# Kernel tuning notes

Measured on AMD Instinct MI355X. Metric: run time of the kernel, lower is better.

The kernel has to match this reference:

```python
import jax, jax.numpy as jnp
import numpy as np
from jax import lax

INPUT, HIDDEN, OUT = 64, 128, 40
B, T = 256, 512


def _lstm_layer(x, Wih, Whh, bih, bhh):
    # x: [B, T, D]; PyTorch gate order: i, f, g, o in stacked [4H, .] weights
    Bsz = x.shape[0]
    H = Whh.shape[1]
    b = bih + bhh

    def step(carry, xt):
        h, c = carry
        gates = xt @ Wih.T + h @ Whh.T + b  # [B, 4H]
        i, f, g, o = jnp.split(gates, 4, axis=-1)
        i = jax.nn.sigmoid(i)
        f = jax.nn.sigmoid(f)
        g = jnp.tanh(g)
        o = jax.nn.sigmoid(o)
        c = f * c + i * g
        h = o * jnp.tanh(c)
        return (h, c), h

    init = (jnp.zeros((Bsz, H), x.dtype), jnp.zeros((Bsz, H), x.dtype))
    (h_last, _), ys = lax.scan(step, init, jnp.swapaxes(x, 0, 1))
    return jnp.swapaxes(ys, 0, 1), h_last


def setup_inputs() -> dict:
    key = jax.random.key(0)
    ks = jax.random.split(key, 11)
    s_in = 1.0 / np.sqrt(HIDDEN)
    u = lambda k, shp: jax.random.uniform(k, shp, jnp.float32, -s_in, s_in)
    return {
        "x": jax.random.normal(ks[0], (B, T, INPUT), jnp.float32),
        "Wih0": u(ks[1], (4 * HIDDEN, INPUT)),
        "Whh0": u(ks[2], (4 * HIDDEN, HIDDEN)),
        "bih0": u(ks[3], (4 * HIDDEN,)),
        "bhh0": u(ks[4], (4 * HIDDEN,)),
        "Wih1": u(ks[5], (4 * HIDDEN, HIDDEN)),
        "Whh1": u(ks[6], (4 * HIDDEN, HIDDEN)),
        "bih1": u(ks[7], (4 * HIDDEN,)),
        "bhh1": u(ks[8], (4 * HIDDEN,)),
        "Wfc": u(ks[9], (OUT, HIDDEN)),
        "bfc": u(ks[10], (OUT,)),
    }


def reference(x, Wih0, Whh0, bih0, bhh0, Wih1, Whh1, bih1, bhh1, Wfc, bfc):
    y0, _ = _lstm_layer(x, Wih0, Whh0, bih0, bhh0)        # [B, T, H]
    _, h_last = _lstm_layer(y0, Wih1, Whh1, bih1, bhh1)   # [B, H] == y[:, -1]
    return h_last @ Wfc.T + bfc                            # [B, 40]
```

## Files before the change

kernel.cpp:

```cpp
#include <hip/hip_runtime.h>

#define BATCH 256
#define TLEN  512
#define DIN   64
#define HID   128
#define NOUT  40

typedef _Float16 f16x8 __attribute__((ext_vector_type(8)));
typedef _Float16 f16x4 __attribute__((ext_vector_type(4)));
typedef float    f32x4 __attribute__((ext_vector_type(4)));

#define MFMA16(a, b, c) __builtin_amdgcn_mfma_f32_16x16x32_f16((a), (b), (c), 0, 0, 0)

#define BARRIER() do {                                      \
    asm volatile("s_waitcnt lgkmcnt(0)" ::: "memory");      \
    __builtin_amdgcn_s_barrier();                           \
} while (0)

static __device__ __forceinline__ f16x8 pack8(float4 a, float4 b) {
    f16x8 v;
    v[0] = (_Float16)a.x; v[1] = (_Float16)a.y; v[2] = (_Float16)a.z; v[3] = (_Float16)a.w;
    v[4] = (_Float16)b.x; v[5] = (_Float16)b.y; v[6] = (_Float16)b.z; v[7] = (_Float16)b.w;
    return v;
}
static __device__ __forceinline__ float sig_(float x) {
    return __builtin_amdgcn_rcpf(1.0f + __expf(-x));
}
static __device__ __forceinline__ float tanh_(float x) {
    return fmaf(-2.0f, __builtin_amdgcn_rcpf(__expf(2.0f * x) + 1.0f), 1.0f);
}

#define LD8(base, g, K, kt) pack8(*(const float4*)((base) + (size_t)(g) * (K) + (kt) * 32 + kg * 8), \
                                  *(const float4*)((base) + (size_t)(g) * (K) + (kt) * 32 + kg * 8 + 4))

__global__ void __attribute__((amdgpu_flat_work_group_size(512, 512), amdgpu_waves_per_eu(2, 2)))
lstm_l0(const float* __restrict__ x,
        const float* __restrict__ Wih, const float* __restrict__ Whh,
        const float* __restrict__ bih, const float* __restrict__ bhh,
        float* __restrict__ hstate, float* __restrict__ cstate,
        _Float16* __restrict__ y0, int t0, int t1)
{
    const int b    = blockIdx.x;
    const int tid  = threadIdx.x;
    const int lane = tid & 63, wave = tid >> 6;
    const int col  = lane & 15, kg = lane >> 4;
    const int hid  = wave * 16 + col;

    __shared__ __align__(16) _Float16 x_lds[2][DIN];
    __shared__ __align__(16) _Float16 h_lds[2][HID];

    f16x8 Wx00 = LD8(Wih, 0 * HID + hid, DIN, 0), Wx01 = LD8(Wih, 0 * HID + hid, DIN, 1);
    f16x8 Wx10 = LD8(Wih, 1 * HID + hid, DIN, 0), Wx11 = LD8(Wih, 1 * HID + hid, DIN, 1);
    f16x8 Wx20 = LD8(Wih, 2 * HID + hid, DIN, 0), Wx21 = LD8(Wih, 2 * HID + hid, DIN, 1);
    f16x8 Wx30 = LD8(Wih, 3 * HID + hid, DIN, 0), Wx31 = LD8(Wih, 3 * HID + hid, DIN, 1);
    f16x8 Wh00 = LD8(Whh, 0 * HID + hid, HID, 0), Wh01 = LD8(Whh, 0 * HID + hid, HID, 1);
    f16x8 Wh02 = LD8(Whh, 0 * HID + hid, HID, 2), Wh03 = LD8(Whh, 0 * HID + hid, HID, 3);
    f16x8 Wh10 = LD8(Whh, 1 * HID + hid, HID, 0), Wh11 = LD8(Whh, 1 * HID + hid, HID, 1);
    f16x8 Wh12 = LD8(Whh, 1 * HID + hid, HID, 2), Wh13 = LD8(Whh, 1 * HID + hid, HID, 3);
    f16x8 Wh20 = LD8(Whh, 2 * HID + hid, HID, 0), Wh21 = LD8(Whh, 2 * HID + hid, HID, 1);
    f16x8 Wh22 = LD8(Whh, 2 * HID + hid, HID, 2), Wh23 = LD8(Whh, 2 * HID + hid, HID, 3);
    f16x8 Wh30 = LD8(Whh, 3 * HID + hid, HID, 0), Wh31 = LD8(Whh, 3 * HID + hid, HID, 1);
    f16x8 Wh32 = LD8(Whh, 3 * HID + hid, HID, 2), Wh33 = LD8(Whh, 3 * HID + hid, HID, 3);
    asm("" : "+a"(Wx00), "+a"(Wx01), "+a"(Wx10), "+a"(Wx11),
             "+a"(Wx20), "+a"(Wx21), "+a"(Wx30), "+a"(Wx31));
    asm("" : "+a"(Wh00), "+a"(Wh01), "+a"(Wh02), "+a"(Wh03),
             "+a"(Wh10), "+a"(Wh11), "+a"(Wh12), "+a"(Wh13));
    asm("" : "+a"(Wh20), "+a"(Wh21), "+a"(Wh22), "+a"(Wh23),
             "+a"(Wh30), "+a"(Wh31), "+a"(Wh32), "+a"(Wh33));

    const float bias0 = bih[0 * HID + hid] + bhh[0 * HID + hid];
    const float bias1 = bih[1 * HID + hid] + bhh[1 * HID + hid];
    const float bias2 = bih[2 * HID + hid] + bhh[2 * HID + hid];
    const float bias3 = bih[3 * HID + hid] + bhh[3 * HID + hid];
    const f32x4 bv0 = {bias0, bias0, bias0, bias0};
    const f32x4 bv1 = {bias1, bias1, bias1, bias1};
    const f32x4 bv2 = {bias2, bias2, bias2, bias2};
    const f32x4 bv3 = {bias3, bias3, bias3, bias3};

    float cc = cstate[(size_t)b * HID + hid];
    float hv = hstate[(size_t)b * HID + hid];
    if (kg == 0) h_lds[0][hid] = (_Float16)hv;

    const float4* xrow = (const float4*)(x + (size_t)b * TLEN * DIN);
    const int lk = tid - 448;
    const bool ldr = ((unsigned)lk < 16u);
    float4 xpfA = make_float4(0, 0, 0, 0), xpfB = xpfA;
    if (ldr) {
        float4 v = xrow[(size_t)t0 * (DIN / 4) + lk];
        f16x4 pw; pw[0] = (_Float16)v.x; pw[1] = (_Float16)v.y;
        pw[2] = (_Float16)v.z; pw[3] = (_Float16)v.w;
        *(f16x4*)&x_lds[0][lk * 4] = pw;
        int ta = t0 + 1 < TLEN ? t0 + 1 : TLEN - 1;
        int tb = t0 + 2 < TLEN ? t0 + 2 : TLEN - 1;
        xpfA = xrow[(size_t)ta * (DIN / 4) + lk];
        xpfB = xrow[(size_t)tb * (DIN / 4) + lk];
    }
    BARRIER();

#define L0_STEP(T, P, XPF) do {                                                  \
    if (ldr) {                                                                   \
        f16x4 pw; pw[0] = (_Float16)XPF.x; pw[1] = (_Float16)XPF.y;              \
        pw[2] = (_Float16)XPF.z; pw[3] = (_Float16)XPF.w;                        \
        *(f16x4*)&x_lds[(P) ^ 1][lk * 4] = pw;                                   \
        int tn = (T) + 3; if (tn > TLEN - 1) tn = TLEN - 1;                      \
        XPF = xrow[(size_t)tn * (DIN / 4) + lk];                                 \
    }                                                                            \
    f16x8 xa0 = *(const f16x8*)&x_lds[P][kg * 8];                                \
    f16x8 xa1 = *(const f16x8*)&x_lds[P][32 + kg * 8];                           \
    f16x8 ha0 = *(const f16x8*)&h_lds[P][kg * 8];                                \
    f16x8 ha1 = *(const f16x8*)&h_lds[P][32 + kg * 8];                           \
    f16x8 ha2 = *(const f16x8*)&h_lds[P][64 + kg * 8];                           \
    f16x8 ha3 = *(const f16x8*)&h_lds[P][96 + kg * 8];                           \
    f32x4 a0 = MFMA16(xa0, Wx00, bv0);                                           \
    f32x4 a1 = MFMA16(xa0, Wx10, bv1);                                           \
    f32x4 a2 = MFMA16(xa0, Wx20, bv2);                                           \
    f32x4 a3 = MFMA16(xa0, Wx30, bv3);                                           \
    a0 = MFMA16(xa1, Wx01, a0); a1 = MFMA16(xa1, Wx11, a1);                      \
    a2 = MFMA16(xa1, Wx21, a2); a3 = MFMA16(xa1, Wx31, a3);                      \
    a0 = MFMA16(ha0, Wh00, a0); a1 = MFMA16(ha0, Wh10, a1);                      \
    a2 = MFMA16(ha0, Wh20, a2); a3 = MFMA16(ha0, Wh30, a3);                      \
    a0 = MFMA16(ha1, Wh01, a0); a1 = MFMA16(ha1, Wh11, a1);                      \
    a2 = MFMA16(ha1, Wh21, a2); a3 = MFMA16(ha1, Wh31, a3);                      \
    a0 = MFMA16(ha2, Wh02, a0); a1 = MFMA16(ha2, Wh12, a1);                      \
    a2 = MFMA16(ha2, Wh22, a2); a3 = MFMA16(ha2, Wh32, a3);                      \
    a0 = MFMA16(ha3, Wh03, a0); a1 = MFMA16(ha3, Wh13, a1);                      \
    a2 = MFMA16(ha3, Wh23, a2); a3 = MFMA16(ha3, Wh33, a3);                      \
    float iv = sig_(a0[0]), fv = sig_(a1[0]);                                    \
    float gv = tanh_(a2[0]), ov = sig_(a3[0]);                                   \
    cc = fmaf(fv, cc, iv * gv);                                                  \
    hv = ov * tanh_(cc);                                                         \
    _Float16 hh = (_Float16)hv;                                                  \
    if (kg == 0) {                                                               \
        h_lds[(P) ^ 1][hid] = hh;                                                \
        y0[((size_t)((T) - t0) * BATCH + b) * HID + hid] = hh;                   \
    }                                                                            \
    BARRIER();                                                                   \
} while (0)

    const int nt = t1 - t0;
    for (int s = 0; s + 1 < nt; s += 2) {
        L0_STEP(t0 + s,     0, xpfA);
        L0_STEP(t0 + s + 1, 1, xpfB);
    }
#undef L0_STEP

    if (kg == 0) {
        cstate[(size_t)b * HID + hid] = cc;
        hstate[(size_t)b * HID + hid] = hv;
    }
}

__global__ void __attribute__((amdgpu_flat_work_group_size(512, 512), amdgpu_waves_per_eu(2, 2)))
lstm_l1(const _Float16* __restrict__ y0in,
        const float* __restrict__ Wih, const float* __restrict__ Whh,
        const float* __restrict__ bih, const float* __restrict__ bhh,
        float* __restrict__ hstate, float* __restrict__ cstate,
        int t0, int t1)
{
    const int b    = blockIdx.x;
    const int tid  = threadIdx.x;
    const int lane = tid & 63, wave = tid >> 6;
    const int col  = lane & 15, kg = lane >> 4;
    const int hid  = wave * 16 + col;

    __shared__ __align__(16) _Float16 y_lds[2][HID];
    __shared__ __align__(16) _Float16 h_lds[2][HID];

    f16x8 Wy00 = LD8(Wih, 0 * HID + hid, HID, 0), Wy01 = LD8(Wih, 0 * HID + hid, HID, 1);
    f16x8 Wy02 = LD8(Wih, 0 * HID + hid, HID, 2), Wy03 = LD8(Wih, 0 * HID + hid, HID, 3);
    f16x8 Wy10 = LD8(Wih, 1 * HID + hid, HID, 0), Wy11 = LD8(Wih, 1 * HID + hid, HID, 1);
    f16x8 Wy12 = LD8(Wih, 1 * HID + hid, HID, 2), Wy13 = LD8(Wih, 1 * HID + hid, HID, 3);
    f16x8 Wy20 = LD8(Wih, 2 * HID + hid, HID, 0), Wy21 = LD8(Wih, 2 * HID + hid, HID, 1);
    f16x8 Wy22 = LD8(Wih, 2 * HID + hid, HID, 2), Wy23 = LD8(Wih, 2 * HID + hid, HID, 3);
    f16x8 Wy30 = LD8(Wih, 3 * HID + hid, HID, 0), Wy31 = LD8(Wih, 3 * HID + hid, HID, 1);
    f16x8 Wy32 = LD8(Wih, 3 * HID + hid, HID, 2), Wy33 = LD8(Wih, 3 * HID + hid, HID, 3);
    f16x8 Wh00 = LD8(Whh, 0 * HID + hid, HID, 0), Wh01 = LD8(Whh, 0 * HID + hid, HID, 1);
    f16x8 Wh02 = LD8(Whh, 0 * HID + hid, HID, 2), Wh03 = LD8(Whh, 0 * HID + hid, HID, 3);
    f16x8 Wh10 = LD8(Whh, 1 * HID + hid, HID, 0), Wh11 = LD8(Whh, 1 * HID + hid, HID, 1);
    f16x8 Wh12 = LD8(Whh, 1 * HID + hid, HID, 2), Wh13 = LD8(Whh, 1 * HID + hid, HID, 3);
    f16x8 Wh20 = LD8(Whh, 2 * HID + hid, HID, 0), Wh21 = LD8(Whh, 2 * HID + hid, HID, 1);
    f16x8 Wh22 = LD8(Whh, 2 * HID + hid, HID, 2), Wh23 = LD8(Whh, 2 * HID + hid, HID, 3);
    f16x8 Wh30 = LD8(Whh, 3 * HID + hid, HID, 0), Wh31 = LD8(Whh, 3 * HID + hid, HID, 1);
    f16x8 Wh32 = LD8(Whh, 3 * HID + hid, HID, 2), Wh33 = LD8(Whh, 3 * HID + hid, HID, 3);
    asm("" : "+a"(Wy00), "+a"(Wy01), "+a"(Wy02), "+a"(Wy03),
             "+a"(Wy10), "+a"(Wy11), "+a"(Wy12), "+a"(Wy13));
    asm("" : "+a"(Wy20), "+a"(Wy21), "+a"(Wy22), "+a"(Wy23),
             "+a"(Wy30), "+a"(Wy31), "+a"(Wy32), "+a"(Wy33));
    asm("" : "+a"(Wh00), "+a"(Wh01), "+a"(Wh02), "+a"(Wh03),
             "+a"(Wh10), "+a"(Wh11), "+a"(Wh12), "+a"(Wh13));
    asm("" : "+a"(Wh20), "+a"(Wh21), "+a"(Wh22), "+a"(Wh23),
             "+a"(Wh30), "+a"(Wh31), "+a"(Wh32), "+a"(Wh33));

    const float bias0 = bih[0 * HID + hid] + bhh[0 * HID + hid];
    const float bias1 = bih[1 * HID + hid] + bhh[1 * HID + hid];
    const float bias2 = bih[2 * HID + hid] + bhh[2 * HID + hid];
    const float bias3 = bih[3 * HID + hid] + bhh[3 * HID + hid];
    const f32x4 bv0 = {bias0, bias0, bias0, bias0};
    const f32x4 bv1 = {bias1, bias1, bias1, bias1};
    const f32x4 bv2 = {bias2, bias2, bias2, bias2};
    const f32x4 bv3 = {bias3, bias3, bias3, bias3};

    float cc = cstate[(size_t)b * HID + hid];
    float hv = hstate[(size_t)b * HID + hid];
    if (kg == 0) h_lds[0][hid] = (_Float16)hv;

    const uint4* yrow = (const uint4*)(y0in);
    const int lk = tid - 448;
    const bool ldr = ((unsigned)lk < 16u);
    const int nt = t1 - t0;
    uint4 ypfA = make_uint4(0, 0, 0, 0), ypfB = ypfA;
    if (ldr) {
        *(uint4*)&y_lds[0][lk * 8] = yrow[((size_t)0 * BATCH + b) * (HID / 8) + lk];
        int ra = 1 < nt - 1 ? 1 : nt - 1;
        int rb = 2 < nt - 1 ? 2 : nt - 1;
        ypfA = yrow[((size_t)ra * BATCH + b) * (HID / 8) + lk];
        ypfB = yrow[((size_t)rb * BATCH + b) * (HID / 8) + lk];
    }
    BARRIER();

#define L1_STEP(REL, P, YPF) do {                                                \
    if (ldr) {                                                                   \
        *(uint4*)&y_lds[(P) ^ 1][lk * 8] = YPF;                                  \
        int rn = (REL) + 3; if (rn > nt - 1) rn = nt - 1;                        \
        YPF = yrow[((size_t)rn * BATCH + b) * (HID / 8) + lk];                   \
    }                                                                            \
    f16x8 ya0 = *(const f16x8*)&y_lds[P][kg * 8];                                \
    f16x8 ya1 = *(const f16x8*)&y_lds[P][32 + kg * 8];                           \
    f16x8 ya2 = *(const f16x8*)&y_lds[P][64 + kg * 8];                           \
    f16x8 ya3 = *(const f16x8*)&y_lds[P][96 + kg * 8];                           \
    f16x8 ha0 = *(const f16x8*)&h_lds[P][kg * 8];                                \
    f16x8 ha1 = *(const f16x8*)&h_lds[P][32 + kg * 8];                           \
    f16x8 ha2 = *(const f16x8*)&h_lds[P][64 + kg * 8];                           \
    f16x8 ha3 = *(const f16x8*)&h_lds[P][96 + kg * 8];                           \
    f32x4 a0 = MFMA16(ya0, Wy00, bv0);                                           \
    f32x4 a1 = MFMA16(ya0, Wy10, bv1);                                           \
    f32x4 a2 = MFMA16(ya0, Wy20, bv2);                                           \
    f32x4 a3 = MFMA16(ya0, Wy30, bv3);                                           \
    a0 = MFMA16(ya1, Wy01, a0); a1 = MFMA16(ya1, Wy11, a1);                      \
    a2 = MFMA16(ya1, Wy21, a2); a3 = MFMA16(ya1, Wy31, a3);                      \
    a0 = MFMA16(ya2, Wy02, a0); a1 = MFMA16(ya2, Wy12, a1);                      \
    a2 = MFMA16(ya2, Wy22, a2); a3 = MFMA16(ya2, Wy32, a3);                      \
    a0 = MFMA16(ya3, Wy03, a0); a1 = MFMA16(ya3, Wy13, a1);                      \
    a2 = MFMA16(ya3, Wy23, a2); a3 = MFMA16(ya3, Wy33, a3);                      \
    a0 = MFMA16(ha0, Wh00, a0); a1 = MFMA16(ha0, Wh10, a1);                      \
    a2 = MFMA16(ha0, Wh20, a2); a3 = MFMA16(ha0, Wh30, a3);                      \
    a0 = MFMA16(ha1, Wh01, a0); a1 = MFMA16(ha1, Wh11, a1);                      \
    a2 = MFMA16(ha1, Wh21, a2); a3 = MFMA16(ha1, Wh31, a3);                      \
    a0 = MFMA16(ha2, Wh02, a0); a1 = MFMA16(ha2, Wh12, a1);                      \
    a2 = MFMA16(ha2, Wh22, a2); a3 = MFMA16(ha2, Wh32, a3);                      \
    a0 = MFMA16(ha3, Wh03, a0); a1 = MFMA16(ha3, Wh13, a1);                      \
    a2 = MFMA16(ha3, Wh23, a2); a3 = MFMA16(ha3, Wh33, a3);                      \
    float iv = sig_(a0[0]), fv = sig_(a1[0]);                                    \
    float gv = tanh_(a2[0]), ov = sig_(a3[0]);                                   \
    cc = fmaf(fv, cc, iv * gv);                                                  \
    hv = ov * tanh_(cc);                                                         \
    if (kg == 0) h_lds[(P) ^ 1][hid] = (_Float16)hv;                             \
    BARRIER();                                                                   \
} while (0)

    for (int s = 0; s + 1 < nt; s += 2) {
        L1_STEP(s,     0, ypfA);
        L1_STEP(s + 1, 1, ypfB);
    }
#undef L1_STEP

    if (kg == 0) {
        cstate[(size_t)b * HID + hid] = cc;
        hstate[(size_t)b * HID + hid] = hv;
    }
}

__global__ __launch_bounds__(128) void fc_kernel(
    const float* __restrict__ h1, const float* __restrict__ Wfc,
    const float* __restrict__ bfc, float* __restrict__ out)
{
    const int b = blockIdx.x;
    const int o = threadIdx.x;
    __shared__ float hs[HID];
    hs[o] = h1[(size_t)b * HID + o];
    __syncthreads();
    if (o < NOUT) {
        const float4* w  = reinterpret_cast<const float4*>(Wfc + (size_t)o * HID);
        const float4* hv = reinterpret_cast<const float4*>(hs);
        float acc = bfc[o];
        #pragma unroll
        for (int q = 0; q < HID / 4; ++q) {
            float4 wv = w[q]; float4 h4 = hv[q];
            acc = fmaf(wv.x, h4.x, fmaf(wv.y, h4.y, fmaf(wv.z, h4.z, fmaf(wv.w, h4.w, acc))));
        }
        out[(size_t)b * NOUT + o] = acc;
    }
}

extern "C" void kernel_launch(void* const* d_in, const int* in_sizes, int n_in,
                              void* d_out, int out_size, void* d_ws, size_t ws_size,
                              hipStream_t stream) {
    const float* x    = (const float*)d_in[0];
    const float* Wih0 = (const float*)d_in[1];
    const float* Whh0 = (const float*)d_in[2];
    const float* bih0 = (const float*)d_in[3];
    const float* bhh0 = (const float*)d_in[4];
    const float* Wih1 = (const float*)d_in[5];
    const float* Whh1 = (const float*)d_in[6];
    const float* bih1 = (const float*)d_in[7];
    const float* bhh1 = (const float*)d_in[8];
    const float* Wfc  = (const float*)d_in[9];
    const float* bfc  = (const float*)d_in[10];
    float* out = (float*)d_out;

    float* hst0 = (float*)d_ws;
    float* cst0 = hst0 + BATCH * HID;
    float* hst1 = cst0 + BATCH * HID;
    float* cst1 = hst1 + BATCH * HID;
    _Float16* y0 = (_Float16*)(cst1 + BATCH * HID);

    const size_t stateBytes = (size_t)4 * BATCH * HID * sizeof(float);
    size_t avail = ws_size > stateBytes ? ws_size - stateBytes : 0;
    int Tc = (int)(avail / ((size_t)BATCH * HID * 2));
    if (Tc > TLEN) Tc = TLEN;
    Tc &= ~1;
    if (Tc < 2) Tc = 2;

    hipMemsetAsync(d_ws, 0, stateBytes, stream);

    for (int t0 = 0; t0 < TLEN; t0 += Tc) {
        int t1 = t0 + Tc; if (t1 > TLEN) t1 = TLEN;
        lstm_l0<<<BATCH, 512, 0, stream>>>(x, Wih0, Whh0, bih0, bhh0, hst0, cst0, y0, t0, t1);
        lstm_l1<<<BATCH, 512, 0, stream>>>(y0, Wih1, Whh1, bih1, bhh1, hst1, cst1, t0, t1);
    }
    fc_kernel<<<BATCH, 128, 0, stream>>>(hst1, Wfc, bfc, out);
}
```

Before: 655.8 us.

## Software-pipeline input projection one step ahead of recurrent MFMA chain

Both LSTM layer kernels now compute the input-to-gate MFMA contribution for step t+1 during step t. The recurrent h-dependent MFMAs start from accumulators that already hold the input term, so the serial dependency chain per step is shorter. The bias is added in scalar form before the activations, and the x/y staging buffers are rotated so the next timestep is already in LDS one step early. Costs are extra accumulator registers and a deeper prefetch pipeline, with changed indexing that could go wrong at chunk boundaries.

```diff
diff --git a/kernel.cpp b/kernel.cpp
--- a/kernel.cpp
+++ b/kernel.cpp
@@ -68,14 +68,11 @@
     asm("" : "+a"(Wh20), "+a"(Wh21), "+a"(Wh22), "+a"(Wh23),
              "+a"(Wh30), "+a"(Wh31), "+a"(Wh32), "+a"(Wh33));
 
-    const float bias0 = bih[0 * HID + hid] + bhh[0 * HID + hid];
-    const float bias1 = bih[1 * HID + hid] + bhh[1 * HID + hid];
-    const float bias2 = bih[2 * HID + hid] + bhh[2 * HID + hid];
-    const float bias3 = bih[3 * HID + hid] + bhh[3 * HID + hid];
-    const f32x4 bv0 = {bias0, bias0, bias0, bias0};
-    const f32x4 bv1 = {bias1, bias1, bias1, bias1};
-    const f32x4 bv2 = {bias2, bias2, bias2, bias2};
-    const f32x4 bv3 = {bias3, bias3, bias3, bias3};
+    const float bs0 = bih[0 * HID + hid] + bhh[0 * HID + hid];
+    const float bs1 = bih[1 * HID + hid] + bhh[1 * HID + hid];
+    const float bs2 = bih[2 * HID + hid] + bhh[2 * HID + hid];
+    const float bs3 = bih[3 * HID + hid] + bhh[3 * HID + hid];
+    const f32x4 z4 = {0.f, 0.f, 0.f, 0.f};
 
     float cc = cstate[(size_t)b * HID + hid];
     float hv = hstate[(size_t)b * HID + hid];
@@ -86,47 +83,61 @@
     const bool ldr = ((unsigned)lk < 16u);
     float4 xpfA = make_float4(0, 0, 0, 0), xpfB = xpfA;
     if (ldr) {
-        float4 v = xrow[(size_t)t0 * (DIN / 4) + lk];
-        f16x4 pw; pw[0] = (_Float16)v.x; pw[1] = (_Float16)v.y;
-        pw[2] = (_Float16)v.z; pw[3] = (_Float16)v.w;
-        *(f16x4*)&x_lds[0][lk * 4] = pw;
-        int ta = t0 + 1 < TLEN ? t0 + 1 : TLEN - 1;
-        int tb = t0 + 2 < TLEN ? t0 + 2 : TLEN - 1;
-        xpfA = xrow[(size_t)ta * (DIN / 4) + lk];
-        xpfB = xrow[(size_t)tb * (DIN / 4) + lk];
+        int g0 = t0,     g1 = t0 + 1, g2 = t0 + 2, g3 = t0 + 3;
+        if (g1 > TLEN - 1) g1 = TLEN - 1;
+        if (g2 > TLEN - 1) g2 = TLEN - 1;
+        if (g3 > TLEN - 1) g3 = TLEN - 1;
+        float4 v0 = xrow[(size_t)g0 * (DIN / 4) + lk];
+        float4 v1 = xrow[(size_t)g1 * (DIN / 4) + lk];
+        f16x4 p;
+        p[0] = (_Float16)v0.x; p[1] = (_Float16)v0.y; p[2] = (_Float16)v0.z; p[3] = (_Float16)v0.w;
+        *(f16x4*)&x_lds[0][lk * 4] = p;
+        p[0] = (_Float16)v1.x; p[1] = (_Float16)v1.y; p[2] = (_Float16)v1.z; p[3] = (_Float16)v1.w;
+        *(f16x4*)&x_lds[1][lk * 4] = p;
+        xpfA = xrow[(size_t)g2 * (DIN / 4) + lk];
+        xpfB = xrow[(size_t)g3 * (DIN / 4) + lk];
     }
     BARRIER();
 
-#define L0_STEP(T, P, XPF) do {                                                  \
+    f32x4 U0, U1, U2, U3, V0, V1, V2, V3;
+    {
+        f16x8 p0 = *(const f16x8*)&x_lds[0][kg * 8];
+        f16x8 p1 = *(const f16x8*)&x_lds[0][32 + kg * 8];
+        U0 = MFMA16(p0, Wx00, z4); U1 = MFMA16(p0, Wx10, z4);
+        U2 = MFMA16(p0, Wx20, z4); U3 = MFMA16(p0, Wx30, z4);
+        U0 = MFMA16(p1, Wx01, U0); U1 = MFMA16(p1, Wx11, U1);
+        U2 = MFMA16(p1, Wx21, U2); U3 = MFMA16(p1, Wx31, U3);
+    }
+    BARRIER();
+
+#define L0_STEP(T, P, XPF, C0, C1, C2, C3, N0, N1, N2, N3) do {                  \
     if (ldr) {                                                                   \
         f16x4 pw; pw[0] = (_Float16)XPF.x; pw[1] = (_Float16)XPF.y;              \
         pw[2] = (_Float16)XPF.z; pw[3] = (_Float16)XPF.w;                        \
-        *(f16x4*)&x_lds[(P) ^ 1][lk * 4] = pw;                                   \
-        int tn = (T) + 3; if (tn > TLEN - 1) tn = TLEN - 1;                      \
+        *(f16x4*)&x_lds[P][lk * 4] = pw;                                         \
+        int tn = (T) + 4; if (tn > TLEN - 1) tn = TLEN - 1;                      \
         XPF = xrow[(size_t)tn * (DIN / 4) + lk];                                 \
     }                                                                            \
-    f16x8 xa0 = *(const f16x8*)&x_lds[P][kg * 8];                                \
-    f16x8 xa1 = *(const f16x8*)&x_lds[P][32 + kg * 8];                           \
     f16x8 ha0 = *(const f16x8*)&h_lds[P][kg * 8];                                \
     f16x8 ha1 = *(const f16x8*)&h_lds[P][32 + kg * 8];                           \
     f16x8 ha2 = *(const f16x8*)&h_lds[P][64 + kg * 8];                           \
     f16x8 ha3 = *(const f16x8*)&h_lds[P][96 + kg * 8];                           \
-    f32x4 a0 = MFMA16(xa0, Wx00, bv0);                                           \
-    f32x4 a1 = MFMA16(xa0, Wx10, bv1);                                           \
-    f32x4 a2 = MFMA16(xa0, Wx20, bv2);                                           \
-    f32x4 a3 = MFMA16(xa0, Wx30, bv3);                                           \
-    a0 = MFMA16(xa1, Wx01, a0); a1 = MFMA16(xa1, Wx11, a1);                      \
-    a2 = MFMA16(xa1, Wx21, a2); a3 = MFMA16(xa1, Wx31, a3);                      \
-    a0 = MFMA16(ha0, Wh00, a0); a1 = MFMA16(ha0, Wh10, a1);                      \
-    a2 = MFMA16(ha0, Wh20, a2); a3 = MFMA16(ha0, Wh30, a3);                      \
+    f16x8 xa0 = *(const f16x8*)&x_lds[(P) ^ 1][kg * 8];                          \
+    f16x8 xa1 = *(const f16x8*)&x_lds[(P) ^ 1][32 + kg * 8];                     \
+    f32x4 a0 = MFMA16(ha0, Wh00, C0), a1 = MFMA16(ha0, Wh10, C1);                \
+    f32x4 a2 = MFMA16(ha0, Wh20, C2), a3 = MFMA16(ha0, Wh30, C3);                \
     a0 = MFMA16(ha1, Wh01, a0); a1 = MFMA16(ha1, Wh11, a1);                      \
     a2 = MFMA16(ha1, Wh21, a2); a3 = MFMA16(ha1, Wh31, a3);                      \
     a0 = MFMA16(ha2, Wh02, a0); a1 = MFMA16(ha2, Wh12, a1);                      \
     a2 = MFMA16(ha2, Wh22, a2); a3 = MFMA16(ha2, Wh32, a3);                      \
     a0 = MFMA16(ha3, Wh03, a0); a1 = MFMA16(ha3, Wh13, a1);                      \
     a2 = MFMA16(ha3, Wh23, a2); a3 = MFMA16(ha3, Wh33, a3);                      \
-    float iv = sig_(a0[0]), fv = sig_(a1[0]);                                    \
-    float gv = tanh_(a2[0]), ov = sig_(a3[0]);                                   \
+    N0 = MFMA16(xa0, Wx00, z4); N1 = MFMA16(xa0, Wx10, z4);                      \
+    N2 = MFMA16(xa0, Wx20, z4); N3 = MFMA16(xa0, Wx30, z4);                      \
+    N0 = MFMA16(xa1, Wx01, N0); N1 = MFMA16(xa1, Wx11, N1);                      \
+    N2 = MFMA16(xa1, Wx21, N2); N3 = MFMA16(xa1, Wx31, N3);                      \
+    float iv = sig_(a0[0] + bs0), fv = sig_(a1[0] + bs1);                        \
+    float gv = tanh_(a2[0] + bs2), ov = sig_(a3[0] + bs3);                       \
     cc = fmaf(fv, cc, iv * gv);                                                  \
     hv = ov * tanh_(cc);                                                         \
     _Float16 hh = (_Float16)hv;                                                  \
@@ -139,8 +150,8 @@
 
     const int nt = t1 - t0;
     for (int s = 0; s + 1 < nt; s += 2) {
-        L0_STEP(t0 + s,     0, xpfA);
-        L0_STEP(t0 + s + 1, 1, xpfB);
+        L0_STEP(t0 + s,     0, xpfA, U0, U1, U2, U3, V0, V1, V2, V3);
+        L0_STEP(t0 + s + 1, 1, xpfB, V0, V1, V2, V3, U0, U1, U2, U3);
     }
 #undef L0_STEP
 
@@ -191,14 +202,11 @@
     asm("" : "+a"(Wh20), "+a"(Wh21), "+a"(Wh22), "+a"(Wh23),
              "+a"(Wh30), "+a"(Wh31), "+a"(Wh32), "+a"(Wh33));
 
-    const float bias0 = bih[0 * HID + hid] + bhh[0 * HID + hid];
-    const float bias1 = bih[1 * HID + hid] + bhh[1 * HID + hid];
-    const float bias2 = bih[2 * HID + hid] + bhh[2 * HID + hid];
-    const float bias3 = bih[3 * HID + hid] + bhh[3 * HID + hid];
-    const f32x4 bv0 = {bias0, bias0, bias0, bias0};
-    const f32x4 bv1 = {bias1, bias1, bias1, bias1};
-    const f32x4 bv2 = {bias2, bias2, bias2, bias2};
-    const f32x4 bv3 = {bias3, bias3, bias3, bias3};
+    const float bs0 = bih[0 * HID + hid] + bhh[0 * HID + hid];
+    const float bs1 = bih[1 * HID + hid] + bhh[1 * HID + hid];
+    const float bs2 = bih[2 * HID + hid] + bhh[2 * HID + hid];
+    const float bs3 = bih[3 * HID + hid] + bhh[3 * HID + hid];
+    const f32x4 z4 = {0.f, 0.f, 0.f, 0.f};
 
     float cc = cstate[(size_t)b * HID + hid];
     float hv = hstate[(size_t)b * HID + hid];
@@ -210,48 +218,65 @@
     const int nt = t1 - t0;
     uint4 ypfA = make_uint4(0, 0, 0, 0), ypfB = ypfA;
     if (ldr) {
+        int i1 = 1 < nt - 1 ? 1 : nt - 1;
+        int i2 = 2 < nt - 1 ? 2 : nt - 1;
+        int i3 = 3 < nt - 1 ? 3 : nt - 1;
         *(uint4*)&y_lds[0][lk * 8] = yrow[((size_t)0 * BATCH + b) * (HID / 8) + lk];
-        int ra = 1 < nt - 1 ? 1 : nt - 1;
-        int rb = 2 < nt - 1 ? 2 : nt - 1;
-        ypfA = yrow[((size_t)ra * BATCH + b) * (HID / 8) + lk];
-        ypfB = yrow[((size_t)rb * BATCH + b) * (HID / 8) + lk];
+        *(uint4*)&y_lds[1][lk * 8] = yrow[((size_t)i1 * BATCH + b) * (HID / 8) + lk];
+        ypfA = yrow[((size_t)i2 * BATCH + b) * (HID / 8) + lk];
+        ypfB = yrow[((size_t)i3 * BATCH + b) * (HID / 8) + lk];
     }
     BARRIER();
 
-#define L1_STEP(REL, P, YPF) do {                                                \
+    f32x4 U0, U1, U2, U3, V0, V1, V2, V3;
+    {
+        f16x8 p0 = *(const f16x8*)&y_lds[0][kg * 8];
+        f16x8 p1 = *(const f16x8*)&y_lds[0][32 + kg * 8];
+        f16x8 p2 = *(const f16x8*)&y_lds[0][64 + kg * 8];
+        f16x8 p3 = *(const f16x8*)&y_lds[0][96 + kg * 8];
+        U0 = MFMA16(p0, Wy00, z4); U1 = MFMA16(p0, Wy10, z4);
+        U2 = MFMA16(p0, Wy20, z4); U3 = MFMA16(p0, Wy30, z4);
+        U0 = MFMA16(p1, Wy01, U0); U1 = MFMA16(p1, Wy11, U1);
+        U2 = MFMA16(p1, Wy21, U2); U3 = MFMA16(p1, Wy31, U3);
+        U0 = MFMA16(p2, Wy02, U0); U1 = MFMA16(p2, Wy12, U1);
+        U2 = MFMA16(p2, Wy22, U2); U3 = MFMA16(p2, Wy32, U3);
+        U0 = MFMA16(p3, Wy03, U0); U1 = MFMA16(p3, Wy13, U1);
+        U2 = MFMA16(p3, Wy23, U2); U3 = MFMA16(p3, Wy33, U3);
+    }
+    BARRIER();
+
+#define L1_STEP(REL, P, YPF, C0, C1, C2, C3, N0, N1, N2, N3) do {                \
     if (ldr) {                                                                   \
-        *(uint4*)&y_lds[(P) ^ 1][lk * 8] = YPF;                                  \
-        int rn = (REL) + 3; if (rn > nt - 1) rn = nt - 1;                        \
+        *(uint4*)&y_lds[P][lk * 8] = YPF;                                        \
+        int rn = (REL) + 4; if (rn > nt - 1) rn = nt - 1;                        \
         YPF = yrow[((size_t)rn * BATCH + b) * (HID / 8) + lk];                   \
     }                                                                            \
-    f16x8 ya0 = *(const f16x8*)&y_lds[P][kg * 8];                                \
-    f16x8 ya1 = *(const f16x8*)&y_lds[P][32 + kg * 8];                           \
-    f16x8 ya2 = *(const f16x8*)&y_lds[P][64 + kg * 8];                           \
-    f16x8 ya3 = *(const f16x8*)&y_lds[P][96 + kg * 8];                           \
     f16x8 ha0 = *(const f16x8*)&h_lds[P][kg * 8];                                \
     f16x8 ha1 = *(const f16x8*)&h_lds[P][32 + kg * 8];                           \
     f16x8 ha2 = *(const f16x8*)&h_lds[P][64 + kg * 8];                           \
     f16x8 ha3 = *(const f16x8*)&h_lds[P][96 + kg * 8];                           \
-    f32x4 a0 = MFMA16(ya0, Wy00, bv0);                                           \
-    f32x4 a1 = MFMA16(ya0, Wy10, bv1);                                           \
-    f32x4 a2 = MFMA16(ya0, Wy20, bv2);                                           \
-    f32x4 a3 = MFMA16(ya0, Wy30, bv3);                                           \
-    a0 = MFMA16(ya1, Wy01, a0); a1 = MFMA16(ya1, Wy11, a1);                      \
-    a2 = MFMA16(ya1, Wy21, a2); a3 = MFMA16(ya1, Wy31, a3);                      \
-    a0 = MFMA16(ya2, Wy02, a0); a1 = MFMA16(ya2, Wy12, a1);                      \
-    a2 = MFMA16(ya2, Wy22, a2); a3 = MFMA16(ya2, Wy32, a3);                      \
-    a0 = MFMA16(ya3, Wy03, a0); a1 = MFMA16(ya3, Wy13, a1);                      \
-    a2 = MFMA16(ya3, Wy23, a2); a3 = MFMA16(ya3, Wy33, a3);                      \
-    a0 = MFMA16(ha0, Wh00, a0); a1 = MFMA16(ha0, Wh10, a1);                      \
-    a2 = MFMA16(ha0, Wh20, a2); a3 = MFMA16(ha0, Wh30, a3);                      \
+    f16x8 ya0 = *(const f16x8*)&y_lds[(P) ^ 1][kg * 8];                          \
+    f16x8 ya1 = *(const f16x8*)&y_lds[(P) ^ 1][32 + kg * 8];                     \
+    f16x8 ya2 = *(const f16x8*)&y_lds[(P) ^ 1][64 + kg * 8];                     \
+    f16x8 ya3 = *(const f16x8*)&y_lds[(P) ^ 1][96 + kg * 8];                     \
+    f32x4 a0 = MFMA16(ha0, Wh00, C0), a1 = MFMA16(ha0, Wh10, C1);                \
+    f32x4 a2 = MFMA16(ha0, Wh20, C2), a3 = MFMA16(ha0, Wh30, C3);                \
     a0 = MFMA16(ha1, Wh01, a0); a1 = MFMA16(ha1, Wh11, a1);                      \
     a2 = MFMA16(ha1, Wh21, a2); a3 = MFMA16(ha1, Wh31, a3);                      \
     a0 = MFMA16(ha2, Wh02, a0); a1 = MFMA16(ha2, Wh12, a1);                      \
     a2 = MFMA16(ha2, Wh22, a2); a3 = MFMA16(ha2, Wh32, a3);                      \
     a0 = MFMA16(ha3, Wh03, a0); a1 = MFMA16(ha3, Wh13, a1);                      \
     a2 = MFMA16(ha3, Wh23, a2); a3 = MFMA16(ha3, Wh33, a3);                      \
-    float iv = sig_(a0[0]), fv = sig_(a1[0]);                                    \
-    float gv = tanh_(a2[0]), ov = sig_(a3[0]);                                   \
+    N0 = MFMA16(ya0, Wy00, z4); N1 = MFMA16(ya0, Wy10, z4);                      \
+    N2 = MFMA16(ya0, Wy20, z4); N3 = MFMA16(ya0, Wy30, z4);                      \
+    N0 = MFMA16(ya1, Wy01, N0); N1 = MFMA16(ya1, Wy11, N1);                      \
+    N2 = MFMA16(ya1, Wy21, N2); N3 = MFMA16(ya1, Wy31, N3);                      \
+    N0 = MFMA16(ya2, Wy02, N0); N1 = MFMA16(ya2, Wy12, N1);                      \
+    N2 = MFMA16(ya2, Wy22, N2); N3 = MFMA16(ya2, Wy32, N3);                      \
+    N0 = MFMA16(ya3, Wy03, N0); N1 = MFMA16(ya3, Wy13, N1);                      \
+    N2 = MFMA16(ya3, Wy23, N2); N3 = MFMA16(ya3, Wy33, N3);                      \
+    float iv = sig_(a0[0] + bs0), fv = sig_(a1[0] + bs1);                        \
+    float gv = tanh_(a2[0] + bs2), ov = sig_(a3[0] + bs3);                       \
     cc = fmaf(fv, cc, iv * gv);                                                  \
     hv = ov * tanh_(cc);                                                         \
     if (kg == 0) h_lds[(P) ^ 1][hid] = (_Float16)hv;                             \
@@ -259,8 +284,8 @@
 } while (0)
 
     for (int s = 0; s + 1 < nt; s += 2) {
-        L1_STEP(s,     0, ypfA);
-        L1_STEP(s + 1, 1, ypfB);
+        L1_STEP(s,     0, ypfA, U0, U1, U2, U3, V0, V1, V2, V3);
+        L1_STEP(s + 1, 1, ypfB, V0, V1, V2, V3, U0, U1, U2, U3);
     }
 #undef L1_STEP
 
```

Result: no change. 650.8 us (-0.8%).
